# Optimization experiments

Measured on AMD Instinct MI355X. Metric: run time of the kernel, lower is better.

The kernel has to match this reference:

```python
import jax, jax.numpy as jnp
import numpy as np

N = 50000
E = 800000
IN_C, HID_C, OUT_C = 256, 128, 64


def setup_inputs() -> dict:
    key = jax.random.key(0)
    k1, k2, k3, k4 = jax.random.split(key, 4)
    x = jax.random.normal(k1, (N, IN_C), dtype=jnp.float32)
    edge_index = jax.random.randint(k2, (2, E), 0, N, dtype=jnp.int64)
    # Glorot-ish init for GCN weights, zero bias (PyG default)
    W1 = jax.random.normal(k3, (IN_C, HID_C), dtype=jnp.float32) / np.sqrt(IN_C)
    b1 = jnp.zeros((HID_C,), dtype=jnp.float32)
    W2 = jax.random.normal(k4, (HID_C, OUT_C), dtype=jnp.float32) / np.sqrt(HID_C)
    b2 = jnp.zeros((OUT_C,), dtype=jnp.float32)
    return {"x": x, "edge_index": edge_index, "W1": W1, "b1": b1, "W2": W2, "b2": b2}


def _gcn_norm(edge_index, num_nodes):
    # Add self-loops, compute symmetric normalization D^-1/2 A D^-1/2 (PyG GCNConv default)
    loops = jnp.arange(num_nodes, dtype=edge_index.dtype)
    src = jnp.concatenate([edge_index[0], loops])  # message sources
    dst = jnp.concatenate([edge_index[1], loops])  # aggregation targets
    deg = jax.ops.segment_sum(jnp.ones_like(dst, dtype=jnp.float32), dst,
                              num_segments=num_nodes)
    dinv = jnp.where(deg > 0, jax.lax.rsqrt(deg), 0.0)
    norm = dinv[src] * dinv[dst]  # [E+N]
    return src, dst, norm


def _gcn_conv(x, W, b, src, dst, norm, num_nodes):
    h = x @ W                                   # [N, out]
    msg = h[src] * norm[:, None]                # gather + scale, [E+N, out]
    out = jax.ops.segment_sum(msg, dst, num_segments=num_nodes)  # scatter-add
    return out + b


def reference(x, edge_index, W1, b1, W2, b2):
    num_nodes = x.shape[0]
    src, dst, norm = _gcn_norm(edge_index, num_nodes)
    h = _gcn_conv(x, W1, b1, src, dst, norm, num_nodes)
    h = jax.nn.relu(h)
    # F.dropout(training=False) -> identity at inference
    return _gcn_conv(h, W2, b2, src, dst, norm, num_nodes)
```

## Files before the change

### kernel.cpp

```cpp
#include <hip/hip_runtime.h>
#include <hip/hip_bf16.h>


typedef __attribute__((ext_vector_type(8))) short short8;
typedef __attribute__((ext_vector_type(4))) float f32x4;

union BF8 {
    short8 s;
    uint4 u;
    __hip_bfloat162 h[4];
};

__device__ __forceinline__ unsigned short f32_to_bf16_rne(float f) {
    unsigned u = __float_as_uint(f);
    return (unsigned short)((u + 0x7fffu + ((u >> 16) & 1u)) >> 16);
}
__device__ __forceinline__ float bf_lo(unsigned v) { return __uint_as_float(v << 16); }
__device__ __forceinline__ float bf_hi(unsigned v) { return __uint_as_float(v & 0xffff0000u); }

__device__ __forceinline__ int xcc_id() {
    int x;
    asm volatile("s_getreg_b32 %0, hwreg(HW_REG_XCC_ID)" : "=s"(x));
    return x & 7;
}

#define ACHUNK 2048
#define BSH 6
#define BN 64
#define CAP 2048
#define CAPS 256
#define NXCD 8

__global__ void wfrag_zero_kernel(const float* __restrict__ W1, const float* __restrict__ W2,
                                  unsigned short* __restrict__ w1f,
                                  unsigned short* __restrict__ w2f,
                                  int* __restrict__ counts, int* __restrict__ bcursor,
                                  int n, int nbk8) {
    int i = blockIdx.x * blockDim.x + threadIdx.x;
    if (i < n) counts[i] = 0;
    if (i < nbk8) bcursor[i] = 0;
    const float* W;
    unsigned short* WF;
    int KS, NCOL, idx;
    if (i < 32768) {
        W = W1; WF = w1f; KS = 8; NCOL = 128; idx = i;
    } else if (i < 32768 + 8192) {
        W = W2; WF = w2f; KS = 4; NCOL = 64; idx = i - 32768;
    } else return;
    int j = idx & 7;
    int lane = (idx >> 3) & 63;
    int f = idx >> 9;
    int ks = f % KS, nt = f / KS;
    int m16 = lane & 15, quad = lane >> 4;
    int ncol = nt * 16 + m16;
    int k = ks * 32 + quad * 8 + j;
    WF[idx] = f32_to_bf16_rne(W[k * NCOL + ncol]);
}

__global__ __launch_bounds__(256) void gemm1_bucket_kernel(
    const float* __restrict__ A, const unsigned short* __restrict__ BFRAG,
    unsigned short* __restrict__ C, int M, int gGemm,
    const int* __restrict__ src, const int* __restrict__ dst,
    int* __restrict__ counts, int* __restrict__ bcursor,
    int2* __restrict__ tmp, int e, int nbk) {
    constexpr int NT = 8, KS = 8;
    constexpr int K = KS * 32;
    constexpr int LSTRIDE = K + 8;
    __shared__ char smem[64 * LSTRIDE * 2];

    const int tid = threadIdx.x;
    if ((int)blockIdx.x < gGemm) {
        unsigned short* Alds = (unsigned short*)smem;
        const int wave = tid >> 6, lane = tid & 63;
        const int quad = lane >> 4, m16 = lane & 15;
        const int rowBase = blockIdx.x * 64;

        constexpr int HALVES = K / 128;
#pragma unroll
        for (int h = 0; h < HALVES; h++) {
            f32x4 v[8];
#pragma unroll
            for (int it = 0; it < 8; it++) {
                int p = (h * 8 + it) * 1024 + tid * 4;
                int rg = rowBase + p / K;
                if (rg >= M) rg = M - 1;
                v[it] = *(const f32x4*)(A + (size_t)rg * K + (p % K));
            }
#pragma unroll
            for (int it = 0; it < 8; it++) {
                int p = (h * 8 + it) * 1024 + tid * 4;
                BF8 cv;
                cv.h[0] = __float22bfloat162_rn(make_float2(v[it].x, v[it].y));
                cv.h[1] = __float22bfloat162_rn(make_float2(v[it].z, v[it].w));
                *(uint2*)&Alds[(p / K) * LSTRIDE + (p % K)] = make_uint2(cv.u.x, cv.u.y);
            }
        }
        __syncthreads();

        const unsigned short* Afrag0 = &Alds[(wave * 16 + m16) * LSTRIDE + quad * 8];
        const uint4* Bfrag = (const uint4*)BFRAG + lane;

        f32x4 acc[NT];
#pragma unroll
        for (int nt = 0; nt < NT; nt++) acc[nt] = f32x4{0.f, 0.f, 0.f, 0.f};
#pragma unroll
        for (int ks = 0; ks < KS; ks++) {
            BF8 af;
            af.u = *(const uint4*)(Afrag0 + ks * 32);
#pragma unroll
            for (int nt = 0; nt < NT; nt++) {
                BF8 bf;
                bf.u = Bfrag[(nt * KS + ks) * 64];
                acc[nt] = __builtin_amdgcn_mfma_f32_16x16x32_bf16(af.s, bf.s, acc[nt], 0, 0, 0);
            }
        }
        const int rowOut = rowBase + wave * 16 + quad * 4;
#pragma unroll
        for (int nt = 0; nt < NT; nt++) {
#pragma unroll
            for (int r = 0; r < 4; r++) {
                int row = rowOut + r;
                if (row < M)
                    C[(size_t)row * 128 + nt * 16 + m16] = f32_to_bf16_rne(acc[nt][r]);
            }
        }
    } else {
        int* sdst = (int*)smem;
        int* hist = (int*)((char*)smem + ACHUNK * 4);
        const int xcd = xcc_id();
        const int b0 = blockIdx.x - gGemm;
        const int start = b0 * ACHUNK;
        const int cnt = min(ACHUNK, e - start);
        for (int t = tid; t < nbk; t += 256) hist[t] = 0;
        __syncthreads();
        for (int i = tid; i < cnt; i += 256) {
            int d = dst[start + i];
            sdst[i] = d;
            atomicAdd(&counts[d], 1);
            atomicAdd(&hist[d >> BSH], 1);
        }
        __syncthreads();
        for (int t = tid; t < nbk; t += 256) {
            int h = hist[t];
            hist[t] = (h > 0) ? atomicAdd(&bcursor[t * NXCD + xcd], h) : 0;
        }
        __syncthreads();
        for (int i = tid; i < cnt; i += 256) {
            int d = sdst[i];
            int slot = atomicAdd(&hist[d >> BSH], 1);
            if (slot < CAPS)
                tmp[((size_t)(d >> BSH) * NXCD + xcd) * CAPS + slot] =
                    make_int2(src[start + i], d);
        }
    }
}

__global__ __launch_bounds__(256) void aggsort_gemm2_kernel(
    const int* __restrict__ counts, const int2* __restrict__ tmp,
    const int* __restrict__ bcursor,
    const unsigned short* __restrict__ hb,
    const float* __restrict__ bias1,
    const unsigned short* __restrict__ w2frag,
    int2* __restrict__ sedge, int2* __restrict__ nodeRange,
    unsigned short* __restrict__ h2, int n) {
    constexpr int LSTRIDE = 136;
    __shared__ int ecnt[BN];
    __shared__ int estart[BN];
    __shared__ int lcur[BN];
    __shared__ float ndinv[BN];
    __shared__ int ssrc[CAP];
    __shared__ float swt[CAP];
    __shared__ unsigned short a1lds[BN * LSTRIDE];

    const int tid = threadIdx.x;
    const int b = blockIdx.x;
    const int nodeBase = b << BSH;
    const int nNodes = min(BN, n - nodeBase);

    int clen[NXCD];
#pragma unroll
    for (int xp = 0; xp < NXCD; xp++) clen[xp] = min(bcursor[b * NXCD + xp], CAPS);

    if (tid < BN) ecnt[tid] = 0;
    __syncthreads();

#pragma unroll
    for (int xp = 0; xp < NXCD; xp++) {
        const int2* sp = tmp + ((size_t)b * NXCD + xp) * CAPS;
        for (int i = tid; i < clen[xp]; i += 256)
            atomicAdd(&ecnt[sp[i].y - nodeBase], 1);
    }
    __syncthreads();

    if (tid < BN) {
        int c = ecnt[tid];
        int x = c;
#pragma unroll
        for (int off = 1; off < 64; off <<= 1) {
            int y = __shfl_up(x, off, 64);
            if (tid >= off) x += y;
        }
        int st = x - c;
        estart[tid] = st;
        lcur[tid] = st;
        ndinv[tid] = rsqrtf((float)c + 1.0f);
        if (tid < nNodes) nodeRange[nodeBase + tid] = make_int2(b * CAP + st, c);
    }
    __syncthreads();

#pragma unroll
    for (int xp = 0; xp < NXCD; xp++) {
        const int2* sp = tmp + ((size_t)b * NXCD + xp) * CAPS;
        for (int i = tid; i < clen[xp]; i += 256) {
            int2 r = sp[i];
            int ln = r.y - nodeBase;
            float w = rsqrtf((float)counts[r.x] + 1.0f) * ndinv[ln];
            int pos = atomicAdd(&lcur[ln], 1);
            ssrc[pos] = r.x;
            swt[pos] = w;
            sedge[(size_t)b * CAP + pos] = make_int2(r.x, __float_as_int(w));
        }
    }
    __syncthreads();

    const int sub = tid & 15;
    const int qw = tid >> 4;
    for (int pass = 0; pass < BN / 16; pass++) {
        int ln = pass * 16 + qw;
        float a0 = 0.f, a1 = 0.f, a2 = 0.f, a3 = 0.f;
        float a4 = 0.f, a5 = 0.f, a6 = 0.f, a7 = 0.f;
        if (ln < nNodes) {
            int node = nodeBase + ln;
            float di = ndinv[ln];
            float d2 = di * di;
            uint4 sv = ((const uint4*)(hb + (size_t)node * 128))[sub];
            a0 = d2 * bf_lo(sv.x); a1 = d2 * bf_hi(sv.x);
            a2 = d2 * bf_lo(sv.y); a3 = d2 * bf_hi(sv.y);
            a4 = d2 * bf_lo(sv.z); a5 = d2 * bf_hi(sv.z);
            a6 = d2 * bf_lo(sv.w); a7 = d2 * bf_hi(sv.w);
            int beg = estart[ln];
            int end = beg + ecnt[ln];
            int i = beg;
            for (; i + 8 <= end; i += 8) {
                int s[8]; float w[8]; uint4 v[8];
#pragma unroll
                for (int j = 0; j < 8; j++) { s[j] = ssrc[i + j]; w[j] = swt[i + j]; }
#pragma unroll
                for (int j = 0; j < 8; j++)
                    v[j] = ((const uint4*)(hb + (size_t)s[j] * 128))[sub];
#pragma unroll
                for (int j = 0; j < 8; j++) {
                    a0 = fmaf(w[j], bf_lo(v[j].x), a0); a1 = fmaf(w[j], bf_hi(v[j].x), a1);
                    a2 = fmaf(w[j], bf_lo(v[j].y), a2); a3 = fmaf(w[j], bf_hi(v[j].y), a3);
                    a4 = fmaf(w[j], bf_lo(v[j].z), a4); a5 = fmaf(w[j], bf_hi(v[j].z), a5);
                    a6 = fmaf(w[j], bf_lo(v[j].w), a6); a7 = fmaf(w[j], bf_hi(v[j].w), a7);
                }
            }
            for (; i + 4 <= end; i += 4) {
                int s[4]; float w[4]; uint4 v[4];
#pragma unroll
                for (int j = 0; j < 4; j++) { s[j] = ssrc[i + j]; w[j] = swt[i + j]; }
#pragma unroll
                for (int j = 0; j < 4; j++)
                    v[j] = ((const uint4*)(hb + (size_t)s[j] * 128))[sub];
#pragma unroll
                for (int j = 0; j < 4; j++) {
                    a0 = fmaf(w[j], bf_lo(v[j].x), a0); a1 = fmaf(w[j], bf_hi(v[j].x), a1);
                    a2 = fmaf(w[j], bf_lo(v[j].y), a2); a3 = fmaf(w[j], bf_hi(v[j].y), a3);
                    a4 = fmaf(w[j], bf_lo(v[j].z), a4); a5 = fmaf(w[j], bf_hi(v[j].z), a5);
                    a6 = fmaf(w[j], bf_lo(v[j].w), a6); a7 = fmaf(w[j], bf_hi(v[j].w), a7);
                }
            }
            for (; i < end; ++i) {
                int s = ssrc[i];
                float w = swt[i];
                uint4 v = ((const uint4*)(hb + (size_t)s * 128))[sub];
                a0 = fmaf(w, bf_lo(v.x), a0); a1 = fmaf(w, bf_hi(v.x), a1);
                a2 = fmaf(w, bf_lo(v.y), a2); a3 = fmaf(w, bf_hi(v.y), a3);
                a4 = fmaf(w, bf_lo(v.z), a4); a5 = fmaf(w, bf_hi(v.z), a5);
                a6 = fmaf(w, bf_lo(v.w), a6); a7 = fmaf(w, bf_hi(v.w), a7);
            }
            float4 b0v = ((const float4*)bias1)[sub * 2];
            float4 b1v = ((const float4*)bias1)[sub * 2 + 1];
            a0 = fmaxf(a0 + b0v.x, 0.f); a1 = fmaxf(a1 + b0v.y, 0.f);
            a2 = fmaxf(a2 + b0v.z, 0.f); a3 = fmaxf(a3 + b0v.w, 0.f);
            a4 = fmaxf(a4 + b1v.x, 0.f); a5 = fmaxf(a5 + b1v.y, 0.f);
            a6 = fmaxf(a6 + b1v.z, 0.f); a7 = fmaxf(a7 + b1v.w, 0.f);
        }
        BF8 p;
        p.h[0] = __float22bfloat162_rn(make_float2(a0, a1));
        p.h[1] = __float22bfloat162_rn(make_float2(a2, a3));
        p.h[2] = __float22bfloat162_rn(make_float2(a4, a5));
        p.h[3] = __float22bfloat162_rn(make_float2(a6, a7));
        *(uint4*)&a1lds[ln * LSTRIDE + sub * 8] = p.u;
    }
    __syncthreads();

    const int wave = tid >> 6, lane = tid & 63;
    const int quad = lane >> 4, m16 = lane & 15;
    const unsigned short* Afrag0 = &a1lds[(wave * 16 + m16) * LSTRIDE + quad * 8];
    const uint4* Bfrag = (const uint4*)w2frag + lane;

    f32x4 acc[4];
#pragma unroll
    for (int nt = 0; nt < 4; nt++) acc[nt] = f32x4{0.f, 0.f, 0.f, 0.f};
#pragma unroll
    for (int ks = 0; ks < 4; ks++) {
        BF8 af;
        af.u = *(const uint4*)(Afrag0 + ks * 32);
#pragma unroll
        for (int nt = 0; nt < 4; nt++) {
            BF8 bf;
            bf.u = Bfrag[(nt * 4 + ks) * 64];
            acc[nt] = __builtin_amdgcn_mfma_f32_16x16x32_bf16(af.s, bf.s, acc[nt], 0, 0, 0);
        }
    }
    const int rowOut = wave * 16 + quad * 4;
#pragma unroll
    for (int nt = 0; nt < 4; nt++) {
#pragma unroll
        for (int r = 0; r < 4; r++) {
            int row = rowOut + r;
            if (row < nNodes)
                h2[(size_t)(nodeBase + row) * 64 + nt * 16 + m16] =
                    f32_to_bf16_rne(acc[nt][r]);
        }
    }
}

__global__ __launch_bounds__(256, 8) void agg64_kernel(
    const int2* __restrict__ nodeRange, const int2* __restrict__ sedge,
    const unsigned short* __restrict__ hb,
    const float* __restrict__ bias, float* __restrict__ out, int n) {
    int node = blockIdx.x * 16 + (threadIdx.x >> 4);
    if (node >= n) return;
    int sub = threadIdx.x & 15;
    int2 nr = nodeRange[node];
    float di = rsqrtf((float)nr.y + 1.0f);
    float d2 = di * di;
    uint2 sv = ((const uint2*)(hb + (size_t)node * 64))[sub];
    float a0 = d2 * bf_lo(sv.x), a1 = d2 * bf_hi(sv.x);
    float a2 = d2 * bf_lo(sv.y), a3 = d2 * bf_hi(sv.y);
    int beg = nr.x, end = nr.x + nr.y;
    int i = beg;
    for (; i + 8 <= end; i += 8) {
        int2 e[8];
        uint2 v[8];
#pragma unroll
        for (int j = 0; j < 8; j++) e[j] = sedge[i + j];
#pragma unroll
        for (int j = 0; j < 8; j++)
            v[j] = ((const uint2*)(hb + (size_t)e[j].x * 64))[sub];
#pragma unroll
        for (int j = 0; j < 8; j++) {
            float w = __int_as_float(e[j].y);
            a0 = fmaf(w, bf_lo(v[j].x), a0); a1 = fmaf(w, bf_hi(v[j].x), a1);
            a2 = fmaf(w, bf_lo(v[j].y), a2); a3 = fmaf(w, bf_hi(v[j].y), a3);
        }
    }
    for (; i + 4 <= end; i += 4) {
        int2 e[4];
        uint2 v[4];
#pragma unroll
        for (int j = 0; j < 4; j++) e[j] = sedge[i + j];
#pragma unroll
        for (int j = 0; j < 4; j++)
            v[j] = ((const uint2*)(hb + (size_t)e[j].x * 64))[sub];
#pragma unroll
        for (int j = 0; j < 4; j++) {
            float w = __int_as_float(e[j].y);
            a0 = fmaf(w, bf_lo(v[j].x), a0); a1 = fmaf(w, bf_hi(v[j].x), a1);
            a2 = fmaf(w, bf_lo(v[j].y), a2); a3 = fmaf(w, bf_hi(v[j].y), a3);
        }
    }
    for (; i < end; ++i) {
        int2 e = sedge[i];
        float w = __int_as_float(e.y);
        uint2 v = ((const uint2*)(hb + (size_t)e.x * 64))[sub];
        a0 = fmaf(w, bf_lo(v.x), a0); a1 = fmaf(w, bf_hi(v.x), a1);
        a2 = fmaf(w, bf_lo(v.y), a2); a3 = fmaf(w, bf_hi(v.y), a3);
    }
    float4 bv = ((const float4*)bias)[sub];
    ((float4*)(out + (size_t)node * 64))[sub] =
        make_float4(a0 + bv.x, a1 + bv.y, a2 + bv.z, a3 + bv.w);
}

extern "C" void kernel_launch(void* const* d_in, const int* in_sizes, int n_in,
                              void* d_out, int out_size, void* d_ws, size_t ws_size,
                              hipStream_t stream) {
    const float* x  = (const float*)d_in[0];
    const int*   ei = (const int*)d_in[1];
    const float* W1 = (const float*)d_in[2];
    const float* b1 = (const float*)d_in[3];
    const float* W2 = (const float*)d_in[4];
    const float* b2 = (const float*)d_in[5];
    float* out = (float*)d_out;

    const int IN_C = 256;
    const int N = in_sizes[0] / IN_C;
    const int E = in_sizes[1] / 2;
    const int* srcA = ei;
    const int* dstA = ei + E;

    char* ws = (char*)d_ws;
    const size_t KB = 1024, MB = 1024 * 1024;
    int*            counts    = (int*)(ws);
    int*            bcursor   = (int*)(ws + 256 * KB);
    unsigned short* w1f       = (unsigned short*)(ws + 1 * MB);
    unsigned short* w2f       = (unsigned short*)(ws + 1 * MB + 64 * KB);
    int2*           tmp       = (int2*)(ws + 2 * MB);
    int2*           sedge     = (int2*)(ws + 16 * MB);
    int2*           nodeRange = (int2*)(ws + 30 * MB);
    unsigned short* h1b       = (unsigned short*)(ws + 31 * MB);
    unsigned short* h2b       = (unsigned short*)(ws + 44 * MB);

    const int NB = (N + BN - 1) / BN;
    const int gGemm = (N + 63) / 64;
    const int nbA = (E + ACHUNK - 1) / ACHUNK;
    const int gWfrag = (max(N, 32768 + 8192) + 255) / 256;

    wfrag_zero_kernel<<<gWfrag, 256, 0, stream>>>(W1, W2, w1f, w2f, counts, bcursor,
                                                  N, NB * NXCD);
    gemm1_bucket_kernel<<<gGemm + nbA, 256, 0, stream>>>(
        x, w1f, h1b, N, gGemm, srcA, dstA, counts, bcursor, tmp, E, NB);
    aggsort_gemm2_kernel<<<NB, 256, 0, stream>>>(
        counts, tmp, bcursor, h1b, b1, w2f, sedge, nodeRange, h2b, N);
    agg64_kernel<<<(N + 15) / 16, 256, 0, stream>>>(nodeRange, sedge, h2b, b2, out, N);
}
```

Before: 206.0 us.

## Replace per-XCD edge buckets with single contiguous buckets and larger chunks

Removes the per-XCD split of the destination-bucket staging area, so each 64-node bucket gets one contiguous CAP-sized region filled through a single global cursor. The bucketing chunk grows from 2048 to 16384 edges per block, which means fewer blocks and fewer global cursor atomics. The dst values are now reread from global memory instead of being staged in LDS. The aggregation kernel reads one contiguous segment instead of eight, and writes sedge coalesced after the local sort. The trade-offs are more contention on the single cursor per bucket, far fewer bucketing blocks (about 49) and therefore less parallelism, and writes to tmp that scatter across the L2 domains of different XCDs.

```diff
diff --git a/kernel.cpp b/kernel.cpp
--- a/kernel.cpp
+++ b/kernel.cpp
@@ -18,27 +18,19 @@
 __device__ __forceinline__ float bf_lo(unsigned v) { return __uint_as_float(v << 16); }
 __device__ __forceinline__ float bf_hi(unsigned v) { return __uint_as_float(v & 0xffff0000u); }
 
-__device__ __forceinline__ int xcc_id() {
-    int x;
-    asm volatile("s_getreg_b32 %0, hwreg(HW_REG_XCC_ID)" : "=s"(x));
-    return x & 7;
-}
-
-#define ACHUNK 2048
+#define ACHUNK 16384
 #define BSH 6
 #define BN 64
 #define CAP 2048
-#define CAPS 256
-#define NXCD 8
 
 __global__ void wfrag_zero_kernel(const float* __restrict__ W1, const float* __restrict__ W2,
                                   unsigned short* __restrict__ w1f,
                                   unsigned short* __restrict__ w2f,
                                   int* __restrict__ counts, int* __restrict__ bcursor,
-                                  int n, int nbk8) {
+                                  int n, int nbk) {
     int i = blockIdx.x * blockDim.x + threadIdx.x;
     if (i < n) counts[i] = 0;
-    if (i < nbk8) bcursor[i] = 0;
+    if (i < nbk) bcursor[i] = 0;
     const float* W;
     unsigned short* WF;
     int KS, NCOL, idx;
@@ -125,32 +117,32 @@
             }
         }
     } else {
-        int* sdst = (int*)smem;
-        int* hist = (int*)((char*)smem + ACHUNK * 4);
-        const int xcd = xcc_id();
+        int* hist = (int*)smem;
+        int* base = hist + 1024;
+        int* cur  = base + 1024;
         const int b0 = blockIdx.x - gGemm;
         const int start = b0 * ACHUNK;
         const int cnt = min(ACHUNK, e - start);
-        for (int t = tid; t < nbk; t += 256) hist[t] = 0;
+        for (int t = tid; t < nbk; t += 256) { hist[t] = 0; cur[t] = 0; }
         __syncthreads();
         for (int i = tid; i < cnt; i += 256) {
             int d = dst[start + i];
-            sdst[i] = d;
             atomicAdd(&counts[d], 1);
             atomicAdd(&hist[d >> BSH], 1);
         }
         __syncthreads();
         for (int t = tid; t < nbk; t += 256) {
             int h = hist[t];
-            hist[t] = (h > 0) ? atomicAdd(&bcursor[t * NXCD + xcd], h) : 0;
+            base[t] = (h > 0) ? atomicAdd(&bcursor[t], h) : 0;
         }
         __syncthreads();
         for (int i = tid; i < cnt; i += 256) {
-            int d = sdst[i];
-            int slot = atomicAdd(&hist[d >> BSH], 1);
-            if (slot < CAPS)
-                tmp[((size_t)(d >> BSH) * NXCD + xcd) * CAPS + slot] =
-                    make_int2(src[start + i], d);
+            int d = dst[start + i];
+            int s = src[start + i];
+            int bk = d >> BSH;
+            int slot = base[bk] + atomicAdd(&cur[bk], 1);
+            if (slot < CAP)
+                tmp[(size_t)bk * CAP + slot] = make_int2(s, d);
         }
     }
 }
@@ -176,20 +168,13 @@
     const int b = blockIdx.x;
     const int nodeBase = b << BSH;
     const int nNodes = min(BN, n - nodeBase);
-
-    int clen[NXCD];
-#pragma unroll
-    for (int xp = 0; xp < NXCD; xp++) clen[xp] = min(bcursor[b * NXCD + xp], CAPS);
+    const int cnt = min(bcursor[b], CAP);
 
     if (tid < BN) ecnt[tid] = 0;
     __syncthreads();
 
-#pragma unroll
-    for (int xp = 0; xp < NXCD; xp++) {
-        const int2* sp = tmp + ((size_t)b * NXCD + xp) * CAPS;
-        for (int i = tid; i < clen[xp]; i += 256)
-            atomicAdd(&ecnt[sp[i].y - nodeBase], 1);
-    }
+    for (int i = tid; i < cnt; i += 256)
+        atomicAdd(&ecnt[tmp[(size_t)b * CAP + i].y - nodeBase], 1);
     __syncthreads();
 
     if (tid < BN) {
@@ -208,20 +193,17 @@
     }
     __syncthreads();
 
-#pragma unroll
-    for (int xp = 0; xp < NXCD; xp++) {
-        const int2* sp = tmp + ((size_t)b * NXCD + xp) * CAPS;
-        for (int i = tid; i < clen[xp]; i += 256) {
-            int2 r = sp[i];
-            int ln = r.y - nodeBase;
-            float w = rsqrtf((float)counts[r.x] + 1.0f) * ndinv[ln];
-            int pos = atomicAdd(&lcur[ln], 1);
-            ssrc[pos] = r.x;
-            swt[pos] = w;
-            sedge[(size_t)b * CAP + pos] = make_int2(r.x, __float_as_int(w));
-        }
+    for (int i = tid; i < cnt; i += 256) {
+        int2 r = tmp[(size_t)b * CAP + i];
+        int ln = r.y - nodeBase;
+        float w = rsqrtf((float)counts[r.x] + 1.0f) * ndinv[ln];
+        int pos = atomicAdd(&lcur[ln], 1);
+        ssrc[pos] = r.x;
+        swt[pos] = w;
     }
     __syncthreads();
+    for (int i = tid; i < cnt; i += 256)
+        sedge[(size_t)b * CAP + i] = make_int2(ssrc[i], __float_as_int(swt[i]));
 
     const int sub = tid & 15;
     const int qw = tid >> 4;
@@ -419,8 +401,7 @@
     const int nbA = (E + ACHUNK - 1) / ACHUNK;
     const int gWfrag = (max(N, 32768 + 8192) + 255) / 256;
 
-    wfrag_zero_kernel<<<gWfrag, 256, 0, stream>>>(W1, W2, w1f, w2f, counts, bcursor,
-                                                  N, NB * NXCD);
+    wfrag_zero_kernel<<<gWfrag, 256, 0, stream>>>(W1, W2, w1f, w2f, counts, bcursor, N, NB);
     gemm1_bucket_kernel<<<gGemm + nbA, 256, 0, stream>>>(
         x, w1f, h1b, N, gGemm, srcA, dstA, counts, bcursor, tmp, E, NB);
     aggsort_gemm2_kernel<<<NB, 256, 0, stream>>>(
```

Result: slower. 227.0 us (+10.2%).
